# Kernel optimization log

Hardware: AMD Instinct MI355X
Metric: run time of the kernel (lower is better)

The kernel has to match this reference:

```python
import jax, jax.numpy as jnp
import numpy as np

HEADS = 12
LN_EPS = 1e-5


def setup_inputs() -> dict:
    B, S, D = 2, 2048, 768
    k = jax.random.key(0)
    ks = jax.random.split(k, 16)
    std = 0.02
    inp = {
        "key": jax.random.normal(ks[0], (B, S, D), jnp.float32),
        "query": jax.random.normal(ks[1], (B, S, D), jnp.float32),
        "value": jax.random.normal(ks[2], (B, S, D), jnp.float32),
        "mask": jax.random.randint(ks[3], (B, S, S), 0, 2).astype(bool),
        "Wk_w": jax.random.normal(ks[4], (D, D), jnp.float32) * std,
        "Wk_b": jnp.zeros((D,), jnp.float32),
        "Wq_w": jax.random.normal(ks[5], (D, D), jnp.float32) * std,
        "Wq_b": jnp.zeros((D,), jnp.float32),
        "Wv_w": jax.random.normal(ks[6], (D, D), jnp.float32) * std,
        "Wv_b": jnp.zeros((D,), jnp.float32),
        "Wc_w": jax.random.normal(ks[7], (D, D), jnp.float32) * std,
        "Wc_b": jnp.zeros((D,), jnp.float32),
        "ln_g": jnp.ones((D,), jnp.float32),
        "ln_b": jnp.zeros((D,), jnp.float32),
    }
    return inp


def _mha(key, query, value, mask, Wk_w, Wk_b, Wq_w, Wq_b, Wv_w, Wv_b,
         Wc_w, Wc_b, ln_g, ln_b):
    B, Sq, D = query.shape
    Sk = key.shape[1]
    H = HEADS
    hd = D // H
    scaler = np.float32(D ** 0.5)  # NOTE: source scales by sqrt(hidden_size), not sqrt(head_dim)

    # QKV projections (torch Linear: x @ W.T + b)
    hk = (key @ Wk_w.T + Wk_b).reshape(B, Sk, H, hd).transpose(2, 0, 1, 3)    # (H,B,Sk,hd)
    hq = (query @ Wq_w.T + Wq_b).reshape(B, Sq, H, hd).transpose(2, 0, 1, 3)  # (H,B,Sq,hd)
    hv = (value @ Wv_w.T + Wv_b).reshape(B, Sk, H, hd).transpose(2, 0, 1, 3)  # (H,B,Sk,hd)

    qk = jnp.einsum('hbqd,hbkd->hbqk', hq, hk) / scaler
    qk = jnp.where(mask[None], -jnp.inf, qk)  # mask repeated over heads in source
    attn = jax.nn.softmax(qk, axis=-1)        # dropout is identity in eval
    out = jnp.einsum('hbqk,hbkd->hbqd', attn, hv)  # (H,B,Sq,hd)

    # Faithful replication of source reshape chain:
    # (H*B,Sq,hd).view(B,H,Sq,hd).permute(1,2,0,3).view(B,Sq,D)
    out = out.reshape(B, H, Sq, hd)             # flat reinterpretation, head-major data
    out = jnp.transpose(out, (1, 2, 0, 3)).reshape(B, Sq, D)

    out = out @ Wc_w.T + Wc_b                   # Wconcat; dropout identity
    x = out + query                             # residual
    mu = jnp.mean(x, axis=-1, keepdims=True)
    var = jnp.mean((x - mu) ** 2, axis=-1, keepdims=True)
    return ln_g * (x - mu) / jnp.sqrt(var + LN_EPS) + ln_b


def reference(key, query, value, mask, Wk_w, Wk_b, Wq_w, Wq_b, Wv_w, Wv_b,
              Wc_w, Wc_b, ln_g, ln_b):
    return _mha(key, query, value, mask, Wk_w, Wk_b, Wq_w, Wq_b,
                Wv_w, Wv_b, Wc_w, Wc_b, ln_g, ln_b)
```

## Files before the change

### kernel.cpp

```cpp
#include <hip/hip_runtime.h>
#include <stdint.h>

typedef float v4f __attribute__((ext_vector_type(4)));
typedef short v8s __attribute__((ext_vector_type(8)));

#define AS1 __attribute__((address_space(1)))
#define AS3 __attribute__((address_space(3)))

__device__ __forceinline__ void load16_to_lds(const void* g, void* l) {
  __builtin_amdgcn_global_load_lds((AS1 void*)g, (AS3 void*)l, 16, 0, 0);
}

__device__ __forceinline__ float fexp2(float x) {
#if __has_builtin(__builtin_amdgcn_exp2f)
  return __builtin_amdgcn_exp2f(x);
#else
  return exp2f(x);
#endif
}

__device__ __forceinline__ unsigned short f2bf_rn(float f) {
  union { float f; uint32_t u; } v; v.f = f;
  return (unsigned short)((v.u + 0x8000u) >> 16);
}
__device__ __forceinline__ uint32_t pack_bf2(float x, float y) {
  union { float f; uint32_t u; } a, b; a.f = x; b.f = y;
  return __builtin_amdgcn_perm(b.u + 0x8000u, a.u + 0x8000u, 0x07060302u);
}

#define QSCALE 0.052058786f

__global__ __launch_bounds__(256) void conv_pack_kernel(
    const float* __restrict__ wk, const float* __restrict__ wq,
    const float* __restrict__ wv, const float* __restrict__ wc,
    const float* __restrict__ kin, const float* __restrict__ qin,
    const float* __restrict__ vin, const uint32_t* __restrict__ mask,
    unsigned short* __restrict__ dk, unsigned short* __restrict__ dq,
    unsigned short* __restrict__ dv, unsigned short* __restrict__ dc,
    unsigned short* __restrict__ dki, unsigned short* __restrict__ dqi,
    unsigned short* __restrict__ dvi, uint32_t* __restrict__ bits) {
  const int id = blockIdx.x;
  const int tid = threadIdx.x;
  if (id >= 11520) {
    const int xx = id - 11520;
    __shared__ int s_i32;
    if (tid == 0) s_i32 = 1;
    __syncthreads();
    if (mask[tid] > 1u) s_i32 = 0;
    __syncthreads();
    if (s_i32) {
      const int lane = tid & 63;
      const int gw = (xx * 256 + tid) >> 6;
#pragma unroll 4
      for (int it = 0; it < 32; ++it) {
        const size_t base = (size_t)gw * 2048 + it * 64;
        unsigned long long bal = __ballot(mask[base + lane] != 0u);
        if (lane == 0) *(unsigned long long*)&bits[base >> 5] = bal;
      }
    } else {
      const int wi = xx * 256 + tid;
      const uint32_t* p = mask + (size_t)wi * 8;
      uint32_t w = 0;
#pragma unroll
      for (int j8 = 0; j8 < 8; ++j8) {
        uint32_t u = p[j8];
#pragma unroll
        for (int k = 0; k < 4; ++k)
          w |= (((u >> (8 * k)) & 0xFFu) ? 1u : 0u) << (j8 * 4 + k);
      }
      bits[wi] = w;
    }
    return;
  }
  const float* s; unsigned short* d; float sc = 1.f; int x;
  if (id < 2304) {
    const int y = id / 576;
    x = id - y * 576;
    if (y == 0)      { s = wk; d = dk; }
    else if (y == 1) { s = wq; d = dq; sc = QSCALE; }
    else if (y == 2) { s = wv; d = dv; }
    else             { s = wc; d = dc; }
  } else {
    const int t = id - 2304;
    const int y = t / 3072;
    x = t - y * 3072;
    if (y == 0)      { s = kin; d = dki; }
    else if (y == 1) { s = qin; d = dqi; }
    else             { s = vin; d = dvi; }
  }
  const int i = x * 256 + tid;
  float4 f = ((const float4*)s)[i];
  uint2 o;
  o.x = pack_bf2(f.x * sc, f.y * sc);
  o.y = pack_bf2(f.z * sc, f.w * sc);
  ((uint2*)d)[i] = o;
}

__global__ __launch_bounds__(256, 3) void gemm_qkv_kernel(
    const unsigned short* __restrict__ qin, const unsigned short* __restrict__ kin,
    const unsigned short* __restrict__ vin,
    const unsigned short* __restrict__ wqb, const unsigned short* __restrict__ wkb,
    const unsigned short* __restrict__ wvb,
    const float* __restrict__ bq, const float* __restrict__ bk,
    const float* __restrict__ bv,
    unsigned short* __restrict__ Qb, unsigned short* __restrict__ Kb,
    unsigned short* __restrict__ Vt) {
  const int which = blockIdx.z;
  const unsigned short* A; const unsigned short* Wb; const float* bias;
  float bscale = 1.f;
  if (which == 0)      { A = qin; Wb = wqb; bias = bq; bscale = QSCALE; }
  else if (which == 1) { A = kin; Wb = wkb; bias = bk; }
  else                 { A = vin; Wb = wvb; bias = bv; }

  const int m0 = blockIdx.x * 128, n0 = blockIdx.y * 128;
  const int tid = threadIdx.x, lane = tid & 63, wid = tid >> 6;
  const int wm = wid >> 1, wn = wid & 1;
  const int l16 = lane & 15, quad = lane >> 4;

  __shared__ __align__(16) unsigned short As[2][128 * 32];
  __shared__ __align__(16) unsigned short Bs[2][128 * 32];

  v4f acc[4][4];
#pragma unroll
  for (int i = 0; i < 4; ++i)
#pragma unroll
    for (int j = 0; j < 4; ++j) { v4f z = {0.f, 0.f, 0.f, 0.f}; acc[i][j] = z; }

  const int c0 = wid * 128 + lane, c1 = wid * 128 + 64 + lane;
  const unsigned short* a0 = A + (size_t)(m0 + (c0 >> 2)) * 768 + (c0 & 3) * 8;
  const unsigned short* a1 = A + (size_t)(m0 + (c1 >> 2)) * 768 + (c1 & 3) * 8;
  const unsigned short* b0 = Wb + (size_t)(n0 + (c0 >> 2)) * 768 + (c0 & 3) * 8;
  const unsigned short* b1 = Wb + (size_t)(n0 + (c1 >> 2)) * 768 + (c1 & 3) * 8;

#define QKV_STAGE(k0, buf)                                         \
  do {                                                             \
    load16_to_lds(a0 + (k0), &As[buf][(wid * 128) * 8]);           \
    load16_to_lds(a1 + (k0), &As[buf][(wid * 128 + 64) * 8]);      \
    load16_to_lds(b0 + (k0), &Bs[buf][(wid * 128) * 8]);           \
    load16_to_lds(b1 + (k0), &Bs[buf][(wid * 128 + 64) * 8]);      \
  } while (0)

  QKV_STAGE(0, 0);
#pragma unroll 2
  for (int ks = 0; ks < 24; ++ks) {
    const int bufc = ks & 1;
    __syncthreads();
    v8s af[4], bf[4];
#pragma unroll
    for (int i = 0; i < 4; ++i)
      af[i] = *(const v8s*)&As[bufc][(wm * 64 + i * 16 + l16) * 32 + quad * 8];
#pragma unroll
    for (int j = 0; j < 4; ++j)
      bf[j] = *(const v8s*)&Bs[bufc][(wn * 64 + j * 16 + l16) * 32 + quad * 8];
    if (ks < 23) QKV_STAGE((ks + 1) * 32, bufc ^ 1);
#pragma unroll
    for (int i = 0; i < 4; ++i)
#pragma unroll
      for (int j = 0; j < 4; ++j)
        acc[i][j] = __builtin_amdgcn_mfma_f32_16x16x32_bf16(af[i], bf[j],
                                                            acc[i][j], 0, 0, 0);
  }
#undef QKV_STAGE

#pragma unroll
  for (int i = 0; i < 4; ++i) {
#pragma unroll
    for (int j = 0; j < 4; ++j) {
      const int mbase = m0 + wm * 64 + i * 16 + quad * 4;
      const int n = n0 + wn * 64 + j * 16 + l16;
      const float bv_ = bias[n] * bscale;
      if (which == 2) {
        const int bb = mbase >> 11, ss = mbase & 2047;
        uint2 pk;
        pk.x = pack_bf2(acc[i][j][0] + bv_, acc[i][j][1] + bv_);
        pk.y = pack_bf2(acc[i][j][2] + bv_, acc[i][j][3] + bv_);
        *(uint2*)&Vt[((size_t)bb * 768 + n) * 2048 + ss] = pk;
      } else {
        unsigned short* dst = (which == 0) ? Qb : Kb;
#pragma unroll
        for (int r = 0; r < 4; ++r)
          dst[(size_t)(mbase + r) * 768 + n] = f2bf_rn(acc[i][j][r] + bv_);
      }
    }
  }
}

__global__ __launch_bounds__(256, 4) void attn_kernel(
    const unsigned short* __restrict__ Qb, const unsigned short* __restrict__ Kb,
    const unsigned short* __restrict__ Vt, const uint32_t* __restrict__ mbits,
    unsigned short* __restrict__ X) {
  const int id = blockIdx.x;
  const int hb = id % 24;
  const int q0 = (id / 24) * 64;
  const int h = hb >> 1, b = hb & 1;
  const int tid = threadIdx.x, w = tid >> 6, lane = tid & 63;
  const int l16 = lane & 15, quad = lane >> 4, l7 = l16 & 7;

  __shared__ __align__(16) unsigned short Kl[2][64 * 64];
  __shared__ __align__(16) unsigned short Vl[2][64 * 64];
  __shared__ __align__(16) unsigned short Pl[4][16 * 64];

  v8s aq[2];
  {
    const unsigned short* qp =
        Qb + (size_t)(b * 2048 + q0 + w * 16 + l16) * 768 + h * 64 + quad * 8;
    aq[0] = *(const v8s*)qp;
    aq[1] = *(const v8s*)(qp + 32);
  }

  v4f o[4], ol;
#pragma unroll
  for (int nt = 0; nt < 4; ++nt) { v4f z = {0.f, 0.f, 0.f, 0.f}; o[nt] = z; }
  { v4f z = {0.f, 0.f, 0.f, 0.f}; ol = z; }

  v8s bones;
  {
    const short v1 = (l16 == 0) ? (short)0x3F80 : (short)0;
#pragma unroll
    for (int j = 0; j < 8; ++j) bones[j] = v1;
  }

  const int rsub = lane >> 3;
  const int csub = ((lane & 7) ^ rsub) * 8;
  const unsigned short* kg0 = Kb + (size_t)(b * 2048 + w * 16) * 768 + h * 64;
  const unsigned short* vg0 = Vt + (size_t)(b * 768 + h * 64 + w * 16) * 2048;
  const uint2* mp =
      (const uint2*)(mbits + (size_t)(b * 2048 + q0 + w * 16 + l16) * 64);

#define ATTN_STAGE(kk0, buf)                                                   \
  do {                                                                         \
    const unsigned short* kg = kg0 + (size_t)(kk0) * 768;                      \
    const unsigned short* vg = vg0 + (kk0);                                    \
    load16_to_lds(kg + (size_t)rsub * 768 + csub, &Kl[buf][(w * 16) * 64]);    \
    load16_to_lds(kg + (size_t)(8 + rsub) * 768 + csub,                        \
                  &Kl[buf][(w * 16 + 8) * 64]);                                \
    load16_to_lds(vg + (size_t)rsub * 2048 + csub, &Vl[buf][(w * 16) * 64]);   \
    load16_to_lds(vg + (size_t)(8 + rsub) * 2048 + csub,                       \
                  &Vl[buf][(w * 16 + 8) * 64]);                                \
  } while (0)

  ATTN_STAGE(0, 0);
  uint2 mreg = mp[0];
#pragma unroll 2
  for (int it = 0; it < 32; ++it) {
    const int bufc = it & 1;
    __syncthreads();

    v8s bk[2][4];
#pragma unroll
    for (int kt = 0; kt < 2; ++kt)
#pragma unroll
      for (int nt = 0; nt < 4; ++nt)
        bk[kt][nt] = *(const v8s*)&Kl[bufc][(nt * 16 + l16) * 64 +
                                           (((kt * 4 + quad) ^ l7) << 3)];
    uint2 mnext;
    if (it < 31) {
      ATTN_STAGE((it + 1) * 64, bufc ^ 1);
      mnext = mp[it + 1];
    }

    v4f sacc[4];
#pragma unroll
    for (int nt = 0; nt < 4; ++nt) { v4f z = {0.f, 0.f, 0.f, 0.f}; sacc[nt] = z; }
#pragma unroll
    for (int kt = 0; kt < 2; ++kt)
#pragma unroll
      for (int nt = 0; nt < 4; ++nt)
        sacc[nt] = __builtin_amdgcn_mfma_f32_16x16x32_bf16(bk[kt][nt], aq[kt],
                                                           sacc[nt], 0, 0, 0);

    const uint32_t u[4] = {mreg.x >> (quad * 4), mreg.x >> (quad * 4 + 16),
                           mreg.y >> (quad * 4), mreg.y >> (quad * 4 + 16)};
#pragma unroll
    for (int nt = 0; nt < 4; ++nt) {
      const float p0 = (u[nt] & 1u) ? 0.f : fexp2(sacc[nt][0]);
      const float p1 = ((u[nt] >> 1) & 1u) ? 0.f : fexp2(sacc[nt][1]);
      const float p2 = ((u[nt] >> 2) & 1u) ? 0.f : fexp2(sacc[nt][2]);
      const float p3 = ((u[nt] >> 3) & 1u) ? 0.f : fexp2(sacc[nt][3]);
      uint2 pk;
      pk.x = pack_bf2(p0, p1);
      pk.y = pack_bf2(p2, p3);
      const int elem =
          l16 * 64 + (((nt * 2 + (quad >> 1)) ^ l7) << 3) + (quad & 1) * 4;
      *(uint2*)&Pl[w][elem] = pk;
    }

#pragma unroll
    for (int kt = 0; kt < 2; ++kt) {
      const v8s ap = *(const v8s*)&Pl[w][l16 * 64 + (((kt * 4 + quad) ^ l7) << 3)];
#pragma unroll
      for (int nt = 0; nt < 4; ++nt) {
        const v8s bv = *(const v8s*)&Vl[bufc][(nt * 16 + l16) * 64 +
                                             (((kt * 4 + quad) ^ l7) << 3)];
        o[nt] = __builtin_amdgcn_mfma_f32_16x16x32_bf16(ap, bv, o[nt], 0, 0, 0);
      }
      ol = __builtin_amdgcn_mfma_f32_16x16x32_bf16(ap, bones, ol, 0, 0, 0);
    }
    mreg = mnext;
  }
#undef ATTN_STAGE

  const int hb2 = 2 * h + b;
  const int b2 = (hb2 >= 12) ? 1 : 0;
  const int h2 = hb2 - 12 * b2;
#pragma unroll
  for (int r = 0; r < 4; ++r) {
    const float lsum = __shfl(ol[r], quad * 16, 64);
    const float inv_l = 1.f / lsum;
    const int q = q0 + w * 16 + quad * 4 + r;
#pragma unroll
    for (int nt = 0; nt < 4; ++nt) {
      const int d = nt * 16 + l16;
      const size_t f = (size_t)h2 * 262144 + (size_t)q * 128 + b2 * 64 + d;
      X[f] = f2bf_rn(o[nt][r] * inv_l);
    }
  }
}

__global__ __launch_bounds__(256, 3) void gemm2_kernel(
    const unsigned short* __restrict__ X, const unsigned short* __restrict__ Wcb,
    const float* __restrict__ bc, const float* __restrict__ query,
    float* __restrict__ out) {
  const int m0 = blockIdx.x * 64, n0 = blockIdx.y * 128;
  const int tid = threadIdx.x, lane = tid & 63, wid = tid >> 6;
  const int wm = wid >> 1, wn = wid & 1;
  const int l16 = lane & 15, quad = lane >> 4;

  __shared__ __align__(16) unsigned short As[2][64 * 32];
  __shared__ __align__(16) unsigned short Bs[2][128 * 32];

  v4f acc[2][4];
#pragma unroll
  for (int i = 0; i < 2; ++i)
#pragma unroll
    for (int j = 0; j < 4; ++j) { v4f z = {0.f, 0.f, 0.f, 0.f}; acc[i][j] = z; }

  const int ca = tid;
  const unsigned short* a0 = X + (size_t)(m0 + (ca >> 2)) * 768 + (ca & 3) * 8;
  const int c0 = wid * 128 + lane, c1 = wid * 128 + 64 + lane;
  const unsigned short* b0 = Wcb + (size_t)(n0 + (c0 >> 2)) * 768 + (c0 & 3) * 8;
  const unsigned short* b1 = Wcb + (size_t)(n0 + (c1 >> 2)) * 768 + (c1 & 3) * 8;

#define G2_STAGE(k0, buf)                                        \
  do {                                                           \
    load16_to_lds(a0 + (k0), &As[buf][(wid * 64) * 8]);          \
    load16_to_lds(b0 + (k0), &Bs[buf][(wid * 128) * 8]);         \
    load16_to_lds(b1 + (k0), &Bs[buf][(wid * 128 + 64) * 8]);    \
  } while (0)

  G2_STAGE(0, 0);
#pragma unroll 2
  for (int ks = 0; ks < 24; ++ks) {
    const int bufc = ks & 1;
    __syncthreads();
    v8s af[2], bf[4];
#pragma unroll
    for (int i = 0; i < 2; ++i)
      af[i] = *(const v8s*)&As[bufc][(wm * 32 + i * 16 + l16) * 32 + quad * 8];
#pragma unroll
    for (int j = 0; j < 4; ++j)
      bf[j] = *(const v8s*)&Bs[bufc][(wn * 64 + j * 16 + l16) * 32 + quad * 8];
    if (ks < 23) G2_STAGE((ks + 1) * 32, bufc ^ 1);
#pragma unroll
    for (int i = 0; i < 2; ++i)
#pragma unroll
      for (int j = 0; j < 4; ++j)
        acc[i][j] = __builtin_amdgcn_mfma_f32_16x16x32_bf16(af[i], bf[j],
                                                            acc[i][j], 0, 0, 0);
  }
#undef G2_STAGE

#pragma unroll
  for (int i = 0; i < 2; ++i) {
#pragma unroll
    for (int j = 0; j < 4; ++j) {
      const int mbase = m0 + wm * 32 + i * 16 + quad * 4;
      const int n = n0 + wn * 64 + j * 16 + l16;
      const float bv_ = bc[n];
#pragma unroll
      for (int r = 0; r < 4; ++r) {
        const int m = mbase + r;
        out[(size_t)m * 768 + n] =
            acc[i][j][r] + bv_ + query[(size_t)m * 768 + n];
      }
    }
  }
}

__global__ __launch_bounds__(256) void ln_kernel(float* __restrict__ out,
                                                 const float* __restrict__ g,
                                                 const float* __restrict__ bta) {
  const int row = blockIdx.x * 4 + (threadIdx.x >> 6);
  const int lane = threadIdx.x & 63;
  float* p = out + (size_t)row * 768 + lane * 12;
  float4 x0 = *(const float4*)(p);
  float4 x1 = *(const float4*)(p + 4);
  float4 x2 = *(const float4*)(p + 8);
  float s = (x0.x + x0.y + x0.z + x0.w) + (x1.x + x1.y + x1.z + x1.w) +
            (x2.x + x2.y + x2.z + x2.w);
  float sq = (x0.x * x0.x + x0.y * x0.y + x0.z * x0.z + x0.w * x0.w) +
             (x1.x * x1.x + x1.y * x1.y + x1.z * x1.z + x1.w * x1.w) +
             (x2.x * x2.x + x2.y * x2.y + x2.z * x2.z + x2.w * x2.w);
#pragma unroll
  for (int off = 1; off < 64; off <<= 1) {
    s += __shfl_xor(s, off, 64);
    sq += __shfl_xor(sq, off, 64);
  }
  const float mu = s * (1.f / 768.f);
  const float var = sq * (1.f / 768.f) - mu * mu;
  const float rstd = rsqrtf(var + 1e-5f);
  const float4 g0 = *(const float4*)(g + lane * 12);
  const float4 g1 = *(const float4*)(g + lane * 12 + 4);
  const float4 g2 = *(const float4*)(g + lane * 12 + 8);
  const float4 b0 = *(const float4*)(bta + lane * 12);
  const float4 b1 = *(const float4*)(bta + lane * 12 + 4);
  const float4 b2 = *(const float4*)(bta + lane * 12 + 8);
  float4 y0, y1, y2;
  y0.x = g0.x * (x0.x - mu) * rstd + b0.x;
  y0.y = g0.y * (x0.y - mu) * rstd + b0.y;
  y0.z = g0.z * (x0.z - mu) * rstd + b0.z;
  y0.w = g0.w * (x0.w - mu) * rstd + b0.w;
  y1.x = g1.x * (x1.x - mu) * rstd + b1.x;
  y1.y = g1.y * (x1.y - mu) * rstd + b1.y;
  y1.z = g1.z * (x1.z - mu) * rstd + b1.z;
  y1.w = g1.w * (x1.w - mu) * rstd + b1.w;
  y2.x = g2.x * (x2.x - mu) * rstd + b2.x;
  y2.y = g2.y * (x2.y - mu) * rstd + b2.y;
  y2.z = g2.z * (x2.z - mu) * rstd + b2.z;
  y2.w = g2.w * (x2.w - mu) * rstd + b2.w;
  *(float4*)(p) = y0;
  *(float4*)(p + 4) = y1;
  *(float4*)(p + 8) = y2;
}

extern "C" void kernel_launch(void* const* d_in, const int* in_sizes, int n_in,
                              void* d_out, int out_size, void* d_ws,
                              size_t ws_size, hipStream_t stream) {
  const float* key   = (const float*)d_in[0];
  const float* query = (const float*)d_in[1];
  const float* value = (const float*)d_in[2];
  const uint32_t* mask = (const uint32_t*)d_in[3];
  const float* Wk = (const float*)d_in[4];
  const float* bk = (const float*)d_in[5];
  const float* Wq = (const float*)d_in[6];
  const float* bq = (const float*)d_in[7];
  const float* Wv = (const float*)d_in[8];
  const float* bv = (const float*)d_in[9];
  const float* Wc = (const float*)d_in[10];
  const float* bc = (const float*)d_in[11];
  const float* lng = (const float*)d_in[12];
  const float* lnb = (const float*)d_in[13];

  char* ws = (char*)d_ws;
  uint32_t*       mbits = (uint32_t*)(ws);
  unsigned short* Wkb = (unsigned short*)(ws + 0x100000);
  unsigned short* Wqb = (unsigned short*)(ws + 0x220000);
  unsigned short* Wvb = (unsigned short*)(ws + 0x340000);
  unsigned short* Wcb = (unsigned short*)(ws + 0x460000);
  unsigned short* Qb  = (unsigned short*)(ws + 0x600000);
  unsigned short* Kb  = (unsigned short*)(ws + 0xC00000);
  unsigned short* Vt  = (unsigned short*)(ws + 0x1200000);
  unsigned short* X   = (unsigned short*)(ws + 0x1800000);
  unsigned short* Kin = (unsigned short*)d_out;
  unsigned short* Qin = (unsigned short*)d_out + 3145728;
  unsigned short* Vin = X;
  float* out = (float*)d_out;

  conv_pack_kernel<<<dim3(12544), dim3(256), 0, stream>>>(
      Wk, Wq, Wv, Wc, key, query, value, mask,
      Wkb, Wqb, Wvb, Wcb, Kin, Qin, Vin, mbits);
  gemm_qkv_kernel<<<dim3(32, 6, 3), dim3(256), 0, stream>>>(
      Qin, Kin, Vin, Wqb, Wkb, Wvb, bq, bk, bv, Qb, Kb, Vt);
  attn_kernel<<<dim3(768), dim3(256), 0, stream>>>(Qb, Kb, Vt, mbits, X);
  gemm2_kernel<<<dim3(64, 6), dim3(256), 0, stream>>>(X, Wcb, bc, query, out);
  ln_kernel<<<dim3(1024), dim3(256), 0, stream>>>(out, lng, lnb);
}
```

Baseline: 240.1 us.

## Give each attention wave two 16-row query tiles to reuse K/V fragments

The attention kernel now runs 2 waves per block instead of 4, and each wave handles 32 query rows as two 16-row sub-tiles. Each K and V fragment read from LDS is reused across both sub-tiles, halving LDS reads per MFMA. Each wave also issues twice as many global-to-LDS loads per stage. The cost is higher register pressure, with launch bounds relaxed to (128,2), and fewer waves to hide latency.

```diff
diff --git a/kernel.cpp b/kernel.cpp
--- a/kernel.cpp
+++ b/kernel.cpp
@@ -185,7 +185,7 @@
   }
 }
 
-__global__ __launch_bounds__(256, 4) void attn_kernel(
+__global__ __launch_bounds__(128, 2) void attn_kernel(
     const unsigned short* __restrict__ Qb, const unsigned short* __restrict__ Kb,
     const unsigned short* __restrict__ Vt, const uint32_t* __restrict__ mbits,
     unsigned short* __restrict__ X) {
@@ -198,20 +198,25 @@
 
   __shared__ __align__(16) unsigned short Kl[2][64 * 64];
   __shared__ __align__(16) unsigned short Vl[2][64 * 64];
-  __shared__ __align__(16) unsigned short Pl[4][16 * 64];
-
-  v8s aq[2];
-  {
+  __shared__ __align__(16) unsigned short Pl[64 * 64];
+
+  v8s aq[2][2];
+#pragma unroll
+  for (int mi = 0; mi < 2; ++mi) {
     const unsigned short* qp =
-        Qb + (size_t)(b * 2048 + q0 + w * 16 + l16) * 768 + h * 64 + quad * 8;
-    aq[0] = *(const v8s*)qp;
-    aq[1] = *(const v8s*)(qp + 32);
-  }
-
-  v4f o[4], ol;
-#pragma unroll
-  for (int nt = 0; nt < 4; ++nt) { v4f z = {0.f, 0.f, 0.f, 0.f}; o[nt] = z; }
-  { v4f z = {0.f, 0.f, 0.f, 0.f}; ol = z; }
+        Qb + (size_t)(b * 2048 + q0 + w * 32 + mi * 16 + l16) * 768 + h * 64 +
+        quad * 8;
+    aq[mi][0] = *(const v8s*)qp;
+    aq[mi][1] = *(const v8s*)(qp + 32);
+  }
+
+  v4f o[2][4], ol[2];
+#pragma unroll
+  for (int mi = 0; mi < 2; ++mi) {
+#pragma unroll
+    for (int nt = 0; nt < 4; ++nt) { v4f z = {0.f, 0.f, 0.f, 0.f}; o[mi][nt] = z; }
+    v4f z = {0.f, 0.f, 0.f, 0.f}; ol[mi] = z;
+  }
 
   v8s bones;
   {
@@ -222,25 +227,27 @@
 
   const int rsub = lane >> 3;
   const int csub = ((lane & 7) ^ rsub) * 8;
-  const unsigned short* kg0 = Kb + (size_t)(b * 2048 + w * 16) * 768 + h * 64;
-  const unsigned short* vg0 = Vt + (size_t)(b * 768 + h * 64 + w * 16) * 2048;
-  const uint2* mp =
-      (const uint2*)(mbits + (size_t)(b * 2048 + q0 + w * 16 + l16) * 64);
-
-#define ATTN_STAGE(kk0, buf)                                                   \
-  do {                                                                         \
-    const unsigned short* kg = kg0 + (size_t)(kk0) * 768;                      \
-    const unsigned short* vg = vg0 + (kk0);                                    \
-    load16_to_lds(kg + (size_t)rsub * 768 + csub, &Kl[buf][(w * 16) * 64]);    \
-    load16_to_lds(kg + (size_t)(8 + rsub) * 768 + csub,                        \
-                  &Kl[buf][(w * 16 + 8) * 64]);                                \
-    load16_to_lds(vg + (size_t)rsub * 2048 + csub, &Vl[buf][(w * 16) * 64]);   \
-    load16_to_lds(vg + (size_t)(8 + rsub) * 2048 + csub,                       \
-                  &Vl[buf][(w * 16 + 8) * 64]);                                \
+  const unsigned short* kg0 = Kb + (size_t)(b * 2048 + w * 32) * 768 + h * 64;
+  const unsigned short* vg0 = Vt + (size_t)(b * 768 + h * 64 + w * 32) * 2048;
+  const uint2* mp0 =
+      (const uint2*)(mbits + (size_t)(b * 2048 + q0 + w * 32 + l16) * 64);
+  const uint2* mp1 =
+      (const uint2*)(mbits + (size_t)(b * 2048 + q0 + w * 32 + 16 + l16) * 64);
+
+#define ATTN_STAGE(kk0, buf)                                              \
+  do {                                                                    \
+    const unsigned short* kg = kg0 + (size_t)(kk0) * 768;                 \
+    const unsigned short* vg = vg0 + (kk0);                               \
+    _Pragma("unroll") for (int j = 0; j < 4; ++j) {                       \
+      load16_to_lds(kg + (size_t)(j * 8 + rsub) * 768 + csub,             \
+                    &Kl[buf][(w * 32 + j * 8) * 64]);                     \
+      load16_to_lds(vg + (size_t)(j * 8 + rsub) * 2048 + csub,            \
+                    &Vl[buf][(w * 32 + j * 8) * 64]);                     \
+    }                                                                     \
   } while (0)
 
   ATTN_STAGE(0, 0);
-  uint2 mreg = mp[0];
+  uint2 mreg[2] = {mp0[0], mp1[0]};
 #pragma unroll 2
   for (int it = 0; it < 32; ++it) {
     const int bufc = it & 1;
@@ -253,50 +260,74 @@
       for (int nt = 0; nt < 4; ++nt)
         bk[kt][nt] = *(const v8s*)&Kl[bufc][(nt * 16 + l16) * 64 +
                                            (((kt * 4 + quad) ^ l7) << 3)];
-    uint2 mnext;
+    uint2 mnext[2];
     if (it < 31) {
       ATTN_STAGE((it + 1) * 64, bufc ^ 1);
-      mnext = mp[it + 1];
-    }
-
-    v4f sacc[4];
-#pragma unroll
-    for (int nt = 0; nt < 4; ++nt) { v4f z = {0.f, 0.f, 0.f, 0.f}; sacc[nt] = z; }
+      mnext[0] = mp0[it + 1];
+      mnext[1] = mp1[it + 1];
+    }
+
+    v4f sacc[2][4];
+#pragma unroll
+    for (int mi = 0; mi < 2; ++mi)
+#pragma unroll
+      for (int nt = 0; nt < 4; ++nt) {
+        v4f z = {0.f, 0.f, 0.f, 0.f};
+        sacc[mi][nt] = z;
+      }
 #pragma unroll
     for (int kt = 0; kt < 2; ++kt)
 #pragma unroll
-      for (int nt = 0; nt < 4; ++nt)
-        sacc[nt] = __builtin_amdgcn_mfma_f32_16x16x32_bf16(bk[kt][nt], aq[kt],
-                                                           sacc[nt], 0, 0, 0);
-
-    const uint32_t u[4] = {mreg.x >> (quad * 4), mreg.x >> (quad * 4 + 16),
-                           mreg.y >> (quad * 4), mreg.y >> (quad * 4 + 16)};
-#pragma unroll
-    for (int nt = 0; nt < 4; ++nt) {
-      const float p0 = (u[nt] & 1u) ? 0.f : fexp2(sacc[nt][0]);
-      const float p1 = ((u[nt] >> 1) & 1u) ? 0.f : fexp2(sacc[nt][1]);
-      const float p2 = ((u[nt] >> 2) & 1u) ? 0.f : fexp2(sacc[nt][2]);
-      const float p3 = ((u[nt] >> 3) & 1u) ? 0.f : fexp2(sacc[nt][3]);
-      uint2 pk;
-      pk.x = pack_bf2(p0, p1);
-      pk.y = pack_bf2(p2, p3);
-      const int elem =
-          l16 * 64 + (((nt * 2 + (quad >> 1)) ^ l7) << 3) + (quad & 1) * 4;
-      *(uint2*)&Pl[w][elem] = pk;
+      for (int mi = 0; mi < 2; ++mi)
+#pragma unroll
+        for (int nt = 0; nt < 4; ++nt)
+          sacc[mi][nt] = __builtin_amdgcn_mfma_f32_16x16x32_bf16(
+              bk[kt][nt], aq[mi][kt], sacc[mi][nt], 0, 0, 0);
+
+#pragma unroll
+    for (int mi = 0; mi < 2; ++mi) {
+      const uint32_t u[4] = {
+          mreg[mi].x >> (quad * 4), mreg[mi].x >> (quad * 4 + 16),
+          mreg[mi].y >> (quad * 4), mreg[mi].y >> (quad * 4 + 16)};
+      const int rowbase = (w * 32 + mi * 16 + l16) * 64;
+#pragma unroll
+      for (int nt = 0; nt < 4; ++nt) {
+        const float p0 = (u[nt] & 1u) ? 0.f : fexp2(sacc[mi][nt][0]);
+        const float p1 = ((u[nt] >> 1) & 1u) ? 0.f : fexp2(sacc[mi][nt][1]);
+        const float p2 = ((u[nt] >> 2) & 1u) ? 0.f : fexp2(sacc[mi][nt][2]);
+        const float p3 = ((u[nt] >> 3) & 1u) ? 0.f : fexp2(sacc[mi][nt][3]);
+        uint2 pk;
+        pk.x = pack_bf2(p0, p1);
+        pk.y = pack_bf2(p2, p3);
+        const int elem =
+            rowbase + (((nt * 2 + (quad >> 1)) ^ l7) << 3) + (quad & 1) * 4;
+        *(uint2*)&Pl[elem] = pk;
+      }
     }
 
 #pragma unroll
     for (int kt = 0; kt < 2; ++kt) {
-      const v8s ap = *(const v8s*)&Pl[w][l16 * 64 + (((kt * 4 + quad) ^ l7) << 3)];
+      v8s ap[2];
+#pragma unroll
+      for (int mi = 0; mi < 2; ++mi)
+        ap[mi] = *(const v8s*)&Pl[(w * 32 + mi * 16 + l16) * 64 +
+                                  (((kt * 4 + quad) ^ l7) << 3)];
 #pragma unroll
       for (int nt = 0; nt < 4; ++nt) {
         const v8s bv = *(const v8s*)&Vl[bufc][(nt * 16 + l16) * 64 +
                                              (((kt * 4 + quad) ^ l7) << 3)];
-        o[nt] = __builtin_amdgcn_mfma_f32_16x16x32_bf16(ap, bv, o[nt], 0, 0, 0);
-      }
-      ol = __builtin_amdgcn_mfma_f32_16x16x32_bf16(ap, bones, ol, 0, 0, 0);
-    }
-    mreg = mnext;
+#pragma unroll
+        for (int mi = 0; mi < 2; ++mi)
+          o[mi][nt] = __builtin_amdgcn_mfma_f32_16x16x32_bf16(ap[mi], bv,
+                                                              o[mi][nt], 0, 0, 0);
+      }
+#pragma unroll
+      for (int mi = 0; mi < 2; ++mi)
+        ol[mi] =
+            __builtin_amdgcn_mfma_f32_16x16x32_bf16(ap[mi], bones, ol[mi], 0, 0, 0);
+    }
+    mreg[0] = mnext[0];
+    mreg[1] = mnext[1];
   }
 #undef ATTN_STAGE
 
@@ -304,15 +335,18 @@
   const int b2 = (hb2 >= 12) ? 1 : 0;
   const int h2 = hb2 - 12 * b2;
 #pragma unroll
-  for (int r = 0; r < 4; ++r) {
-    const float lsum = __shfl(ol[r], quad * 16, 64);
-    const float inv_l = 1.f / lsum;
-    const int q = q0 + w * 16 + quad * 4 + r;
-#pragma unroll
-    for (int nt = 0; nt < 4; ++nt) {
-      const int d = nt * 16 + l16;
-      const size_t f = (size_t)h2 * 262144 + (size_t)q * 128 + b2 * 64 + d;
-      X[f] = f2bf_rn(o[nt][r] * inv_l);
+  for (int mi = 0; mi < 2; ++mi) {
+#pragma unroll
+    for (int r = 0; r < 4; ++r) {
+      const float lsum = __shfl(ol[mi][r], quad * 16, 64);
+      const float inv_l = 1.f / lsum;
+      const int q = q0 + w * 32 + mi * 16 + quad * 4 + r;
+#pragma unroll
+      for (int nt = 0; nt < 4; ++nt) {
+        const int d = nt * 16 + l16;
+        const size_t f = (size_t)h2 * 262144 + (size_t)q * 128 + b2 * 64 + d;
+        X[f] = f2bf_rn(o[mi][nt][r] * inv_l);
+      }
     }
   }
 }
@@ -471,7 +505,7 @@
       Wkb, Wqb, Wvb, Wcb, Kin, Qin, Vin, mbits);
   gemm_qkv_kernel<<<dim3(32, 6, 3), dim3(256), 0, stream>>>(
       Qin, Kin, Vin, Wqb, Wkb, Wvb, bq, bk, bv, Qb, Kb, Vt);
-  attn_kernel<<<dim3(768), dim3(256), 0, stream>>>(Qb, Kb, Vt, mbits, X);
+  attn_kernel<<<dim3(768), dim3(128), 0, stream>>>(Qb, Kb, Vt, mbits, X);
   gemm2_kernel<<<dim3(64, 6), dim3(256), 0, stream>>>(X, Wcb, bc, query, out);
   ln_kernel<<<dim3(1024), dim3(256), 0, stream>>>(out, lng, lnb);
 }
```

Measured after the change: 245.6 us. +2.3%, slower.
